# Kernel optimization log

Measured on AMD Instinct MI355X. Metric: run time of the kernel, lower is better.

## Reference

```python
import jax, jax.numpy as jnp
import numpy as np

E = 1024      # hidden_size
H = 16        # num_attention_heads
HD = E // H   # head_dim
EPS = 1e-5


def _mw_linear(x, Wt, bt, Wi, bi, split):
    # multiway linear: text weights on tokens [:split], image weights on [split:]
    xt = x[:, :split] @ Wt.T + bt
    xi = x[:, split:] @ Wi.T + bi
    return jnp.concatenate([xt, xi], axis=1)


def _ln(x, g, b):
    mu = jnp.mean(x, axis=-1, keepdims=True)
    var = jnp.mean(jnp.square(x - mu), axis=-1, keepdims=True)
    return (x - mu) * jax.lax.rsqrt(var + EPS) * g + b


def _mw_ln(x, gt, bt, gi, bi, split):
    return jnp.concatenate([_ln(x[:, :split], gt, bt), _ln(x[:, split:], gi, bi)], axis=1)


def setup_inputs() -> dict:
    key = jax.random.key(0)
    ks = jax.random.split(key, 24)
    B, T = 8, 1024
    d = {
        'query': jax.random.normal(ks[0], (B, T, E), jnp.float32),
        'key': jax.random.normal(ks[1], (B, T, E), jnp.float32),
        'value': jax.random.normal(ks[2], (B, T, E), jnp.float32),
        'attention_mask': jax.random.normal(ks[3], (T, T), jnp.float32) * 0.02,
    }
    i = 4
    for name in ['q', 'k', 'v', 'o']:
        d[f'W{name}_t'] = jax.random.normal(ks[i], (E, E), jnp.float32) * 0.02; i += 1
        d[f'b{name}_t'] = jnp.zeros((E,), jnp.float32)
        d[f'W{name}_i'] = jax.random.normal(ks[i], (E, E), jnp.float32) * 0.02; i += 1
        d[f'b{name}_i'] = jnp.zeros((E,), jnp.float32)
    d['ln_g_t'] = jnp.ones((E,), jnp.float32)
    d['ln_b_t'] = jnp.zeros((E,), jnp.float32)
    d['ln_g_i'] = jnp.ones((E,), jnp.float32)
    d['ln_b_i'] = jnp.zeros((E,), jnp.float32)
    d['split_position'] = 64
    return d


def reference(query, key, value, attention_mask,
              Wq_t, bq_t, Wq_i, bq_i,
              Wk_t, bk_t, Wk_i, bk_i,
              Wv_t, bv_t, Wv_i, bv_i,
              Wo_t, bo_t, Wo_i, bo_i,
              ln_g_t, ln_b_t, ln_g_i, ln_b_i,
              split_position):
    B, T, _ = query.shape
    S = key.shape[1]
    scaling = HD ** -0.5
    q = _mw_linear(query, Wq_t, bq_t, Wq_i, bq_i, split_position) * scaling
    k = _mw_linear(key, Wk_t, bk_t, Wk_i, bk_i, split_position)
    v = _mw_linear(value, Wv_t, bv_t, Wv_i, bv_i, split_position)
    q = q.reshape(B, T, H, HD)
    k = k.reshape(B, S, H, HD)
    v = v.reshape(B, S, H, HD)
    # [B, H, T, S] attention logits
    attn_weights = jnp.einsum('bthd,bshd->bhts', q, k)
    attn_weights = jnp.nan_to_num(attn_weights) + attention_mask[None, None]
    probs = jax.nn.softmax(attn_weights.astype(jnp.float32), axis=-1).astype(attn_weights.dtype)
    attn = jnp.einsum('bhts,bshd->bthd', probs, v).reshape(B, T, E)
    attn = _mw_ln(attn, ln_g_t, ln_b_t, ln_g_i, ln_b_i, split_position)
    attn = _mw_linear(attn, Wo_t, bo_t, Wo_i, bo_i, split_position)
    return attn
```

## Files before the change

kernel.cpp:

```cpp
#include <hip/hip_runtime.h>

#define E_DIM 1024
#define HEADS 16
#define HD 64
#define LOG2E 1.44269504088896340736f

typedef unsigned short ushort_t;
typedef __attribute__((ext_vector_type(8))) short bf16x8;
typedef __attribute__((ext_vector_type(4))) float floatx4;
typedef __attribute__((ext_vector_type(4))) float f32x4;
typedef __attribute__((ext_vector_type(16))) float floatx16;

__device__ inline unsigned int pack2bf(float a, float b) {
    unsigned int ua = __builtin_bit_cast(unsigned int, a);
    unsigned int ub = __builtin_bit_cast(unsigned int, b);
    ua = (ua + 0x8000u) >> 16;
    ub = (ub + 0x8000u) & 0xFFFF0000u;
    return ua | ub;
}
__device__ inline unsigned short f2bf(float a) {
    return (unsigned short)((__builtin_bit_cast(unsigned int, a) + 0x8000u) >> 16);
}
__device__ inline float bf2f(unsigned int s) {
    return __builtin_bit_cast(float, s << 16);
}

__device__ __forceinline__ void load_lds16(const void* g, void* l) {
    __builtin_amdgcn_global_load_lds(
        (const __attribute__((address_space(1))) unsigned int*)g,
        (__attribute__((address_space(3))) unsigned int*)l, 16, 0, 0);
}

__global__ __launch_bounds__(256) void cvt_inputs(
    const float* s0, const float* s1, const float* s2,
    ushort_t* d0, ushort_t* d1, ushort_t* d2)
{
    const float* __restrict__ src = (blockIdx.y == 0) ? s0 : (blockIdx.y == 1) ? s1 : s2;
    ushort_t* __restrict__ dst = (blockIdx.y == 0) ? d0 : (blockIdx.y == 1) ? d1 : d2;
    size_t i = ((size_t)blockIdx.x * 256 + threadIdx.x) * 8;
    float4 a = *(const float4*)&src[i];
    float4 b = *(const float4*)&src[i + 4];
    uint4 o;
    o.x = pack2bf(a.x, a.y); o.y = pack2bf(a.z, a.w);
    o.z = pack2bf(b.x, b.y); o.w = pack2bf(b.z, b.w);
    *(uint4*)&dst[i] = o;
}

__global__ __launch_bounds__(256) void cvt_weights(
    const float* w0, const float* w1, const float* w2, const float* w3,
    const float* w4, const float* w5, const float* w6, const float* w7,
    ushort_t* __restrict__ out)
{
    const float* srcs[8] = {w0, w1, w2, w3, w4, w5, w6, w7};
    const float* __restrict__ src = srcs[blockIdx.y];
    ushort_t* __restrict__ dst = out + (size_t)blockIdx.y * E_DIM * E_DIM;
    size_t i = ((size_t)blockIdx.x * 256 + threadIdx.x) * 8;
    float4 a = *(const float4*)&src[i];
    float4 b = *(const float4*)&src[i + 4];
    uint4 o;
    o.x = pack2bf(a.x, a.y); o.y = pack2bf(a.z, a.w);
    o.z = pack2bf(b.x, b.y); o.w = pack2bf(b.z, b.w);
    *(uint4*)&dst[i] = o;
}

__global__ __launch_bounds__(256) void mask_pack(
    const float* __restrict__ m, float* __restrict__ mp, int T_)
{
    int gid = blockIdx.x * 256 + threadIdx.x;
    int t  = gid >> 8;
    int s4 = (gid & 255) * 4;
    float4 v = *(const float4*)&m[(size_t)t * T_ + s4];
    int qt = t >> 5, q32 = t & 31;
    int it = s4 >> 6, s6 = s4 & 63;
    int j = s6 >> 5, up = (s6 >> 3) & 3, hi = (s6 >> 2) & 1;
    int L = j * 4 + up, lane = q32 + 32 * hi;
    size_t o = (((size_t)(qt * 16 + it) * 8 + L) * 64 + lane) * 4;
    float4 ov;
    ov.x = v.x * LOG2E - 16.0f; ov.y = v.y * LOG2E - 16.0f;
    ov.z = v.z * LOG2E - 16.0f; ov.w = v.w * LOG2E - 16.0f;
    *(float4*)&mp[o] = ov;
}

template<bool OUT_BF16>
__device__ __forceinline__ void gemm_core(
    const ushort_t* __restrict__ x, const ushort_t* __restrict__ W,
    const float* __restrict__ bias, void* __restrict__ outv,
    int m0, int n0, int split, int kind, float scale, int T_)
{
    __shared__ __align__(16) ushort_t As[2][128 * 32];
    __shared__ __align__(16) ushort_t Bs[2][128 * 32];

    const int tid  = threadIdx.x;
    const int lane = tid & 63;
    const int wv   = tid >> 6;
    const int rw   = (wv >> 1) * 64;
    const int cw   = (wv & 1) * 64;
    const int am   = lane & 15;
    const int aq   = lane >> 4;

    const int grow = wv * 32 + (lane >> 2);
    const int gcol = ((lane & 3) ^ ((lane >> 3) & 3)) * 8;
    const int akey = ((am >> 1) & 3) * 8;

    floatx4 acc[4][4];
    #pragma unroll
    for (int i = 0; i < 4; ++i)
        #pragma unroll
        for (int j = 0; j < 4; ++j)
            acc[i][j] = (floatx4){0.f, 0.f, 0.f, 0.f};

    load_lds16(&x[(size_t)(m0 + grow) * E_DIM + gcol],      &As[0][(wv * 32) * 32]);
    load_lds16(&x[(size_t)(m0 + grow + 16) * E_DIM + gcol], &As[0][(wv * 32 + 16) * 32]);
    load_lds16(&W[(size_t)(n0 + grow) * E_DIM + gcol],      &Bs[0][(wv * 32) * 32]);
    load_lds16(&W[(size_t)(n0 + grow + 16) * E_DIM + gcol], &Bs[0][(wv * 32 + 16) * 32]);
    __syncthreads();

    for (int k0 = 0; k0 < E_DIM; k0 += 32) {
        const int cur = (k0 >> 5) & 1;
        if (k0 + 32 < E_DIM) {
            const int nxt = cur ^ 1;
            const int kn  = k0 + 32;
            load_lds16(&x[(size_t)(m0 + grow) * E_DIM + kn + gcol],      &As[nxt][(wv * 32) * 32]);
            load_lds16(&x[(size_t)(m0 + grow + 16) * E_DIM + kn + gcol], &As[nxt][(wv * 32 + 16) * 32]);
            load_lds16(&W[(size_t)(n0 + grow) * E_DIM + kn + gcol],      &Bs[nxt][(wv * 32) * 32]);
            load_lds16(&W[(size_t)(n0 + grow + 16) * E_DIM + kn + gcol], &Bs[nxt][(wv * 32 + 16) * 32]);
        }

        bf16x8 af[4], bfv[4];
        #pragma unroll
        for (int i = 0; i < 4; ++i)
            af[i] = *(const bf16x8*)&As[cur][(rw + i * 16 + am) * 32 + ((aq * 8) ^ akey)];
        #pragma unroll
        for (int j = 0; j < 4; ++j)
            bfv[j] = *(const bf16x8*)&Bs[cur][(cw + j * 16 + am) * 32 + ((aq * 8) ^ akey)];

        #pragma unroll
        for (int i = 0; i < 4; ++i)
            #pragma unroll
            for (int j = 0; j < 4; ++j)
                acc[i][j] = __builtin_amdgcn_mfma_f32_16x16x32_bf16(af[i], bfv[j], acc[i][j], 0, 0, 0);

        __syncthreads();
    }

    const int cq = lane >> 4;
    const int cm = lane & 15;
    const int t0m = m0 % T_;
    #pragma unroll
    for (int j = 0; j < 4; ++j) {
        int n = n0 + cw + j * 16 + cm;
        float bv = bias[n];
        #pragma unroll
        for (int i = 0; i < 4; ++i) {
            int mbase = m0 + rw + i * 16 + cq * 4;
            int tbase = t0m + rw + i * 16 + cq * 4;
            #pragma unroll
            for (int r = 0; r < 4; ++r) {
                int m = mbase + r;
                int t = tbase + r;
                if (((t < split) ? 0 : 1) != kind) continue;
                float val = (acc[i][j][r] + bv) * scale;
                if (OUT_BF16) ((ushort_t*)outv)[(size_t)m * E_DIM + n] = f2bf(val);
                else          ((float*)outv)[(size_t)m * E_DIM + n] = val;
            }
        }
    }
}

__device__ __forceinline__ int gemm_pick_m0(int kind, int split, int T_, bool& ok)
{
    ok = true;
    if (kind == 0) {
        const int nq = (split + 127) >> 7;
        const int Bb = (int)(gridDim.x * 128) / T_;
        if ((int)blockIdx.x >= Bb * nq) { ok = false; return 0; }
        const int batch = blockIdx.x / nq, tq = blockIdx.x % nq;
        return batch * T_ + tq * 128;
    }
    const int m0 = blockIdx.x * 128;
    if ((m0 % T_) + 128 <= split) { ok = false; return 0; }
    return m0;
}

__global__ __launch_bounds__(256) void gemm_qkv(
    const ushort_t* __restrict__ xq, const ushort_t* __restrict__ xk,
    const ushort_t* __restrict__ xv, const ushort_t* __restrict__ wall,
    const float* bq_t, const float* bq_i, const float* bk_t, const float* bk_i,
    const float* bv_t, const float* bv_i,
    ushort_t* oq, ushort_t* ok, ushort_t* ov,
    const int* __restrict__ split_ptr, int T_)
{
    const int split = *split_ptr;
    const int z = blockIdx.z;
    const int op = z >> 1;
    const int kind = z & 1;
    const int n0 = blockIdx.y * 128;

    bool ok2;
    const int m0 = gemm_pick_m0(kind, split, T_, ok2);
    if (!ok2) return;

    const ushort_t* x = (op == 0) ? xq : (op == 1) ? xk : xv;
    ushort_t* outp    = (op == 0) ? oq : (op == 1) ? ok : ov;
    const ushort_t* W = wall + (size_t)z * E_DIM * E_DIM;
    const float* bias = (op == 0) ? (kind ? bq_i : bq_t)
                      : (op == 1) ? (kind ? bk_i : bk_t)
                                  : (kind ? bv_i : bv_t);
    float scale = (op == 0) ? 0.125f * LOG2E : 1.0f;

    gemm_core<true>(x, W, bias, outp, m0, n0, split, kind, scale, T_);
}

__global__ __launch_bounds__(256) void gemm_o(
    const ushort_t* __restrict__ x, const ushort_t* __restrict__ Wt,
    const float* bt, const ushort_t* __restrict__ Wi, const float* bi,
    float* __restrict__ outp, const int* __restrict__ split_ptr, int T_)
{
    const int split = *split_ptr;
    const int kind = blockIdx.z;
    const int n0 = blockIdx.y * 128;

    bool ok2;
    const int m0 = gemm_pick_m0(kind, split, T_, ok2);
    if (!ok2) return;

    gemm_core<false>(x, kind ? Wi : Wt, kind ? bi : bt, outp, m0, n0, split, kind, 1.0f, T_);
}

__global__ __launch_bounds__(256) void attn_mfma32(
    const ushort_t* __restrict__ q, const ushort_t* __restrict__ k,
    const ushort_t* __restrict__ v, const float* __restrict__ maskP,
    ushort_t* __restrict__ outp, int T_)
{
    const int tid  = threadIdx.x;
    const int lane = tid & 63;
    const int wv   = tid >> 6;
    const int b    = blockIdx.x;
    const int h    = blockIdx.y;
    const int r0   = blockIdx.z * 128;

    const int q32 = lane & 31;
    const int hi  = lane >> 5;

    __shared__ __align__(16) ushort_t Ks[64 * 72];
    __shared__ __align__(16) ushort_t VT[64 * 72];

    const int qrow = r0 + wv * 32 + q32;
    const int qt16 = ((r0 >> 5) + wv) * 16;

    bf16x8 aqf[4];
    #pragma unroll
    for (int dc = 0; dc < 4; ++dc)
        aqf[dc] = *(const bf16x8*)&q[((size_t)(b * T_ + qrow)) * E_DIM + h * HD + dc * 16 + hi * 8];

    floatx16 oa[2];
    #pragma unroll
    for (int n = 0; n < 2; ++n)
        #pragma unroll
        for (int i = 0; i < 16; ++i) oa[n][i] = 0.f;
    float lsum = 0.f;

    const int kr = tid >> 2;
    const int kc = (tid & 3) * 16;
    const int vr = (tid >> 4) * 4;
    const int vc = (tid & 15) * 4;

    uint4 kreg[2];
    uint2 vreg[4];

    kreg[0] = *(const uint4*)&k[((size_t)(b * T_ + kr)) * E_DIM + h * HD + kc];
    kreg[1] = *(const uint4*)&k[((size_t)(b * T_ + kr)) * E_DIM + h * HD + kc + 8];
    #pragma unroll
    for (int i = 0; i < 4; ++i)
        vreg[i] = *(const uint2*)&v[((size_t)(b * T_ + vr + i)) * E_DIM + h * HD + vc];

    *(uint4*)&Ks[kr * 72 + kc]     = kreg[0];
    *(uint4*)&Ks[kr * 72 + kc + 8] = kreg[1];
    {
        const ushort_t* vp = (const ushort_t*)vreg;
        #pragma unroll
        for (int t = 0; t < 4; ++t) {
            uint2 w;
            w.x = (unsigned int)vp[0 * 4 + t] | ((unsigned int)vp[1 * 4 + t] << 16);
            w.y = (unsigned int)vp[2 * 4 + t] | ((unsigned int)vp[3 * 4 + t] << 16);
            *(uint2*)&VT[(vc + t) * 72 + vr] = w;
        }
    }
    __syncthreads();

    const int NT = T_ / 64;
    #pragma unroll 1
    for (int it = 0; it < NT; ++it) {
        const int s0 = it * 64;

        if (it + 1 < NT) {
            const int sn = s0 + 64;
            kreg[0] = *(const uint4*)&k[((size_t)(b * T_ + sn + kr)) * E_DIM + h * HD + kc];
            kreg[1] = *(const uint4*)&k[((size_t)(b * T_ + sn + kr)) * E_DIM + h * HD + kc + 8];
            #pragma unroll
            for (int i = 0; i < 4; ++i)
                vreg[i] = *(const uint2*)&v[((size_t)(b * T_ + sn + vr + i)) * E_DIM + h * HD + vc];
        }

        f32x4 mk[8];
        {
            const float* mp = maskP + ((size_t)(qt16 + it) << 11) + (lane << 2);
            #pragma unroll
            for (int L = 0; L < 8; ++L)
                mk[L] = *(const f32x4*)&mp[L << 8];
        }

        floatx16 sa[2];
        #pragma unroll
        for (int j = 0; j < 2; ++j)
            #pragma unroll
            for (int i = 0; i < 16; ++i) sa[j][i] = 0.f;
        __builtin_amdgcn_s_setprio(1);
        #pragma unroll
        for (int j = 0; j < 2; ++j)
            #pragma unroll
            for (int dc = 0; dc < 4; ++dc) {
                bf16x8 kf = *(const bf16x8*)&Ks[(32 * j + q32) * 72 + dc * 16 + hi * 8];
                sa[j] = __builtin_amdgcn_mfma_f32_32x32x16_bf16(kf, aqf[dc], sa[j], 0, 0, 0);
            }
        __builtin_amdgcn_s_setprio(0);

        float lp0 = 0.f, lp1 = 0.f, lp2 = 0.f, lp3 = 0.f;
        #pragma unroll
        for (int j = 0; j < 2; ++j)
            #pragma unroll
            for (int i = 0; i < 16; ++i) {
                float e = exp2f(sa[j][i] + mk[(j << 2) | (i >> 2)][i & 3]);
                sa[j][i] = e;
                if ((i & 3) == 0) lp0 += e;
                else if ((i & 3) == 1) lp1 += e;
                else if ((i & 3) == 2) lp2 += e;
                else lp3 += e;
            }
        lsum += (lp0 + lp1) + (lp2 + lp3);

        unsigned int W[2][8], X[2][8];
        #pragma unroll
        for (int j = 0; j < 2; ++j)
            #pragma unroll
            for (int u = 0; u < 8; ++u)
                W[j][u] = pack2bf(sa[j][2 * u], sa[j][2 * u + 1]);
        #pragma unroll
        for (int j = 0; j < 2; ++j)
            #pragma unroll
            for (int u = 0; u < 8; ++u)
                X[j][u] = (unsigned int)__shfl_xor((int)W[j][u], 32, 64);

        __builtin_amdgcn_s_setprio(1);
        #pragma unroll
        for (int s = 0; s < 4; ++s) {
            const int j = s >> 1;
            const int hh = (s & 1) * 4;
            union { unsigned int u[4]; bf16x8 v8; } pf;
            pf.u[0] = hi ? X[j][hh + 2] : W[j][hh + 0];
            pf.u[1] = hi ? X[j][hh + 3] : W[j][hh + 1];
            pf.u[2] = hi ? W[j][hh + 2] : X[j][hh + 0];
            pf.u[3] = hi ? W[j][hh + 3] : X[j][hh + 1];
            #pragma unroll
            for (int n = 0; n < 2; ++n) {
                bf16x8 vf = *(const bf16x8*)&VT[(n * 32 + q32) * 72 + s * 16 + hi * 8];
                oa[n] = __builtin_amdgcn_mfma_f32_32x32x16_bf16(pf.v8, vf, oa[n], 0, 0, 0);
            }
        }
        __builtin_amdgcn_s_setprio(0);

        if (it + 1 < NT) {
            __syncthreads();
            *(uint4*)&Ks[kr * 72 + kc]     = kreg[0];
            *(uint4*)&Ks[kr * 72 + kc + 8] = kreg[1];
            const ushort_t* vp = (const ushort_t*)vreg;
            #pragma unroll
            for (int t = 0; t < 4; ++t) {
                uint2 w;
                w.x = (unsigned int)vp[0 * 4 + t] | ((unsigned int)vp[1 * 4 + t] << 16);
                w.y = (unsigned int)vp[2 * 4 + t] | ((unsigned int)vp[3 * 4 + t] << 16);
                *(uint2*)&VT[(vc + t) * 72 + vr] = w;
            }
            __syncthreads();
        }
    }

    lsum += __shfl_xor(lsum, 32, 64);
    float inv = 1.0f / lsum;
    #pragma unroll
    for (int i = 0; i < 16; ++i) {
        int qi = (i & 3) + 8 * (i >> 2) + 4 * hi;
        float vi = __shfl(inv, qi + (lane & 32), 64);
        size_t orow = ((size_t)(b * T_ + r0 + wv * 32 + qi)) * E_DIM + h * HD;
        outp[orow + q32]      = f2bf(oa[0][i] * vi);
        outp[orow + 32 + q32] = f2bf(oa[1][i] * vi);
    }
}

__global__ __launch_bounds__(256) void mw_ln_bf16(
    const ushort_t* __restrict__ x,
    const float* __restrict__ gt, const float* __restrict__ bt,
    const float* __restrict__ gi, const float* __restrict__ bi,
    ushort_t* __restrict__ out,
    const int* __restrict__ split_ptr, int T_)
{
    const int split = *split_ptr;
    const int row = blockIdx.x;
    const int t = row % T_;
    const float* __restrict__ g  = (t < split) ? gt : gi;
    const float* __restrict__ bb = (t < split) ? bt : bi;

    const int tid = threadIdx.x;
    const int lane = tid & 63;
    const int wid = tid >> 6;

    __shared__ float red[8];

    uint2 xv = *(const uint2*)&x[(size_t)row * E_DIM + tid * 4];
    float f0 = bf2f(xv.x & 0xffffu), f1 = bf2f(xv.x >> 16);
    float f2 = bf2f(xv.y & 0xffffu), f3 = bf2f(xv.y >> 16);
    float s = f0 + f1 + f2 + f3;
    #pragma unroll
    for (int off = 1; off < 64; off <<= 1) s += __shfl_xor(s, off, 64);
    if (lane == 0) red[wid] = s;
    __syncthreads();
    float mu = (red[0] + red[1] + red[2] + red[3]) * (1.0f / E_DIM);

    float d0 = f0 - mu, d1 = f1 - mu, d2 = f2 - mu, d3 = f3 - mu;
    float s2 = d0*d0 + d1*d1 + d2*d2 + d3*d3;
    #pragma unroll
    for (int off = 1; off < 64; off <<= 1) s2 += __shfl_xor(s2, off, 64);
    if (lane == 0) red[4 + wid] = s2;
    __syncthreads();
    float var = (red[4] + red[5] + red[6] + red[7]) * (1.0f / E_DIM);
    float rstd = rsqrtf(var + 1e-5f);

    float4 gv = *(const float4*)&g[tid * 4];
    float4 bv = *(const float4*)&bb[tid * 4];
    uint2 ov;
    ov.x = pack2bf(d0 * rstd * gv.x + bv.x, d1 * rstd * gv.y + bv.y);
    ov.y = pack2bf(d2 * rstd * gv.z + bv.z, d3 * rstd * gv.w + bv.w);
    *(uint2*)&out[(size_t)row * E_DIM + tid * 4] = ov;
}

extern "C" void kernel_launch(void* const* d_in, const int* in_sizes, int n_in,
                              void* d_out, int out_size, void* d_ws, size_t ws_size,
                              hipStream_t stream) {
    const float* query = (const float*)d_in[0];
    const float* key   = (const float*)d_in[1];
    const float* value = (const float*)d_in[2];
    const float* mask  = (const float*)d_in[3];
    const float* Wq_t = (const float*)d_in[4];  const float* bq_t = (const float*)d_in[5];
    const float* Wq_i = (const float*)d_in[6];  const float* bq_i = (const float*)d_in[7];
    const float* Wk_t = (const float*)d_in[8];  const float* bk_t = (const float*)d_in[9];
    const float* Wk_i = (const float*)d_in[10]; const float* bk_i = (const float*)d_in[11];
    const float* Wv_t = (const float*)d_in[12]; const float* bv_t = (const float*)d_in[13];
    const float* Wv_i = (const float*)d_in[14]; const float* bv_i = (const float*)d_in[15];
    const float* Wo_t = (const float*)d_in[16]; const float* bo_t = (const float*)d_in[17];
    const float* Wo_i = (const float*)d_in[18]; const float* bo_i = (const float*)d_in[19];
    const float* ln_g_t = (const float*)d_in[20]; const float* ln_b_t = (const float*)d_in[21];
    const float* ln_g_i = (const float*)d_in[22]; const float* ln_b_i = (const float*)d_in[23];
    const int* split = (const int*)d_in[24];

    float* out = (float*)d_out;

    const int BT = in_sizes[0] / E_DIM;
    const int T_ = 1024;
    const int B  = BT / T_;

    ushort_t* ws = (ushort_t*)d_ws;
    const size_t nx = (size_t)BT * E_DIM;
    const size_t nw = (size_t)E_DIM * E_DIM;
    ushort_t* xq_bf = ws;
    ushort_t* xk_bf = ws + nx;
    ushort_t* xv_bf = ws + 2 * nx;
    ushort_t* k_bf  = ws + 3 * nx;
    ushort_t* v_bf  = ws + 4 * nx;
    ushort_t* w_bf  = ws + 5 * nx;
    ushort_t* q_bf  = (ushort_t*)d_out;
    float* maskP    = (float*)xk_bf;

    dim3 blk(256);
    const int cvt_blocks = (int)(nx / 2048);
    const int wcvt_blocks = (int)(nw / 2048);

    cvt_weights<<<dim3(wcvt_blocks, 8), blk, 0, stream>>>(
        Wq_t, Wq_i, Wk_t, Wk_i, Wv_t, Wv_i, Wo_t, Wo_i, w_bf);
    cvt_inputs<<<dim3(cvt_blocks, 3), blk, 0, stream>>>(
        query, key, value, xq_bf, xk_bf, xv_bf);

    gemm_qkv<<<dim3(BT / 128, E_DIM / 128, 6), blk, 0, stream>>>(
        xq_bf, xk_bf, xv_bf, w_bf,
        bq_t, bq_i, bk_t, bk_i, bv_t, bv_i,
        q_bf, k_bf, v_bf, split, T_);

    mask_pack<<<dim3(T_ * T_ / 4 / 256), blk, 0, stream>>>(mask, maskP, T_);

    attn_mfma32<<<dim3(B, HEADS, T_ / 128), blk, 0, stream>>>(
        q_bf, k_bf, v_bf, maskP, q_bf, T_);

    mw_ln_bf16<<<dim3(BT), blk, 0, stream>>>(
        q_bf, ln_g_t, ln_b_t, ln_g_i, ln_b_i, xq_bf, split, T_);

    gemm_o<<<dim3(BT / 128, E_DIM / 128, 2), blk, 0, stream>>>(
        xq_bf, w_bf + 6 * nw, bo_t, w_bf + 7 * nw, bo_i, out, split, T_);
}
```

Measured before the change: 478.2 us.

## Fuse Q, K and V projections into a single GEMM block

Replaces the per-projection QKV GEMM (grid z=6) with one kernel in which each block computes the Q, K and V tiles for the same rows and columns. It keeps three accumulator sets and stages all three operand pairs into 96KB of dynamic LDS with double buffering. The aim is fewer blocks and shared index and launch setup. The cost is much higher register and LDS use per block, which lowers occupancy, and the three projections share no input data to reuse.

```diff
diff --git a/kernel.cpp b/kernel.cpp
--- a/kernel.cpp
+++ b/kernel.cpp
@@ -81,6 +81,135 @@
     *(float4*)&mp[o] = ov;
 }
 
+__device__ __forceinline__ int gemm_pick_m0(int kind, int split, int T_, bool& ok)
+{
+    ok = true;
+    if (kind == 0) {
+        const int nq = (split + 127) >> 7;
+        const int Bb = (int)(gridDim.x * 128) / T_;
+        if ((int)blockIdx.x >= Bb * nq) { ok = false; return 0; }
+        const int batch = blockIdx.x / nq, tq = blockIdx.x % nq;
+        return batch * T_ + tq * 128;
+    }
+    const int m0 = blockIdx.x * 128;
+    if ((m0 % T_) + 128 <= split) { ok = false; return 0; }
+    return m0;
+}
+
+__global__ __launch_bounds__(256) void gemm_qkv_f(
+    const ushort_t* __restrict__ xq, const ushort_t* __restrict__ xk,
+    const ushort_t* __restrict__ xv, const ushort_t* __restrict__ wall,
+    const float* bq_t, const float* bq_i, const float* bk_t, const float* bk_i,
+    const float* bv_t, const float* bv_i,
+    ushort_t* oq, ushort_t* ok, ushort_t* ov,
+    const int* __restrict__ split_ptr, int T_)
+{
+    extern __shared__ __align__(16) ushort_t sh[];
+
+    const int split = *split_ptr;
+    const int kind = blockIdx.z;
+    const int n0 = blockIdx.y * 128;
+    bool ok2;
+    const int m0 = gemm_pick_m0(kind, split, T_, ok2);
+    if (!ok2) return;
+
+    const int tid  = threadIdx.x;
+    const int lane = tid & 63;
+    const int wv   = tid >> 6;
+    const int rw   = (wv >> 1) * 64;
+    const int cw   = (wv & 1) * 64;
+    const int am   = lane & 15;
+    const int aq   = lane >> 4;
+
+    const int grow = wv * 32 + (lane >> 2);
+    const int gcol = ((lane & 3) ^ ((lane >> 3) & 3)) * 8;
+    const int akey = ((am >> 1) & 3) * 8;
+
+    const ushort_t* xp[3] = { xq, xk, xv };
+    const ushort_t* Wp[3] = { wall + (size_t)(0 * 2 + kind) * E_DIM * E_DIM,
+                              wall + (size_t)(1 * 2 + kind) * E_DIM * E_DIM,
+                              wall + (size_t)(2 * 2 + kind) * E_DIM * E_DIM };
+
+    ushort_t* As = sh;
+    ushort_t* Bs = sh + 24576;
+
+    floatx4 acc[3][4][4];
+    #pragma unroll
+    for (int op = 0; op < 3; ++op)
+        #pragma unroll
+        for (int i = 0; i < 4; ++i)
+            #pragma unroll
+            for (int j = 0; j < 4; ++j)
+                acc[op][i][j] = (floatx4){0.f, 0.f, 0.f, 0.f};
+
+    auto stage_all = [&](int kn, int buf) {
+        #pragma unroll
+        for (int op = 0; op < 3; ++op) {
+            ushort_t* a = As + (op * 2 + buf) * 4096;
+            ushort_t* b = Bs + (op * 2 + buf) * 4096;
+            load_lds16(&xp[op][(size_t)(m0 + grow) * E_DIM + kn + gcol],      &a[(wv * 32) * 32]);
+            load_lds16(&xp[op][(size_t)(m0 + grow + 16) * E_DIM + kn + gcol], &a[(wv * 32 + 16) * 32]);
+            load_lds16(&Wp[op][(size_t)(n0 + grow) * E_DIM + kn + gcol],      &b[(wv * 32) * 32]);
+            load_lds16(&Wp[op][(size_t)(n0 + grow + 16) * E_DIM + kn + gcol], &b[(wv * 32 + 16) * 32]);
+        }
+    };
+
+    stage_all(0, 0);
+    __syncthreads();
+
+    for (int k0 = 0; k0 < E_DIM; k0 += 32) {
+        const int cur = (k0 >> 5) & 1;
+        if (k0 + 32 < E_DIM)
+            stage_all(k0 + 32, cur ^ 1);
+
+        #pragma unroll
+        for (int op = 0; op < 3; ++op) {
+            const ushort_t* a = As + (op * 2 + cur) * 4096;
+            const ushort_t* b = Bs + (op * 2 + cur) * 4096;
+            bf16x8 af[4], bfv[4];
+            #pragma unroll
+            for (int i = 0; i < 4; ++i)
+                af[i] = *(const bf16x8*)&a[(rw + i * 16 + am) * 32 + ((aq * 8) ^ akey)];
+            #pragma unroll
+            for (int j = 0; j < 4; ++j)
+                bfv[j] = *(const bf16x8*)&b[(cw + j * 16 + am) * 32 + ((aq * 8) ^ akey)];
+            #pragma unroll
+            for (int i = 0; i < 4; ++i)
+                #pragma unroll
+                for (int j = 0; j < 4; ++j)
+                    acc[op][i][j] = __builtin_amdgcn_mfma_f32_16x16x32_bf16(af[i], bfv[j], acc[op][i][j], 0, 0, 0);
+        }
+        __syncthreads();
+    }
+
+    const int cq = lane >> 4;
+    const int cm = lane & 15;
+    const int t0m = m0 % T_;
+    const float* biases[3] = { kind ? bq_i : bq_t, kind ? bk_i : bk_t, kind ? bv_i : bv_t };
+    ushort_t* outs[3] = { oq, ok, ov };
+    #pragma unroll
+    for (int op = 0; op < 3; ++op) {
+        const float scale = (op == 0) ? 0.125f * LOG2E : 1.0f;
+        ushort_t* outp = outs[op];
+        #pragma unroll
+        for (int j = 0; j < 4; ++j) {
+            int n = n0 + cw + j * 16 + cm;
+            float bv = biases[op][n];
+            #pragma unroll
+            for (int i = 0; i < 4; ++i) {
+                int mbase = m0 + rw + i * 16 + cq * 4;
+                int tbase = t0m + rw + i * 16 + cq * 4;
+                #pragma unroll
+                for (int r = 0; r < 4; ++r) {
+                    int t = tbase + r;
+                    if (((t < split) ? 0 : 1) != kind) continue;
+                    outp[(size_t)(mbase + r) * E_DIM + n] = f2bf((acc[op][i][j][r] + bv) * scale);
+                }
+            }
+        }
+    }
+}
+
 template<bool OUT_BF16>
 __device__ __forceinline__ void gemm_core(
     const ushort_t* __restrict__ x, const ushort_t* __restrict__ W,
@@ -165,50 +294,6 @@
             }
         }
     }
-}
-
-__device__ __forceinline__ int gemm_pick_m0(int kind, int split, int T_, bool& ok)
-{
-    ok = true;
-    if (kind == 0) {
-        const int nq = (split + 127) >> 7;
-        const int Bb = (int)(gridDim.x * 128) / T_;
-        if ((int)blockIdx.x >= Bb * nq) { ok = false; return 0; }
-        const int batch = blockIdx.x / nq, tq = blockIdx.x % nq;
-        return batch * T_ + tq * 128;
-    }
-    const int m0 = blockIdx.x * 128;
-    if ((m0 % T_) + 128 <= split) { ok = false; return 0; }
-    return m0;
-}
-
-__global__ __launch_bounds__(256) void gemm_qkv(
-    const ushort_t* __restrict__ xq, const ushort_t* __restrict__ xk,
-    const ushort_t* __restrict__ xv, const ushort_t* __restrict__ wall,
-    const float* bq_t, const float* bq_i, const float* bk_t, const float* bk_i,
-    const float* bv_t, const float* bv_i,
-    ushort_t* oq, ushort_t* ok, ushort_t* ov,
-    const int* __restrict__ split_ptr, int T_)
-{
-    const int split = *split_ptr;
-    const int z = blockIdx.z;
-    const int op = z >> 1;
-    const int kind = z & 1;
-    const int n0 = blockIdx.y * 128;
-
-    bool ok2;
-    const int m0 = gemm_pick_m0(kind, split, T_, ok2);
-    if (!ok2) return;
-
-    const ushort_t* x = (op == 0) ? xq : (op == 1) ? xk : xv;
-    ushort_t* outp    = (op == 0) ? oq : (op == 1) ? ok : ov;
-    const ushort_t* W = wall + (size_t)z * E_DIM * E_DIM;
-    const float* bias = (op == 0) ? (kind ? bq_i : bq_t)
-                      : (op == 1) ? (kind ? bk_i : bk_t)
-                                  : (kind ? bv_i : bv_t);
-    float scale = (op == 0) ? 0.125f * LOG2E : 1.0f;
-
-    gemm_core<true>(x, W, bias, outp, m0, n0, split, kind, scale, T_);
 }
 
 __global__ __launch_bounds__(256) void gemm_o(
@@ -489,7 +574,7 @@
     cvt_inputs<<<dim3(cvt_blocks, 3), blk, 0, stream>>>(
         query, key, value, xq_bf, xk_bf, xv_bf);
 
-    gemm_qkv<<<dim3(BT / 128, E_DIM / 128, 6), blk, 0, stream>>>(
+    gemm_qkv_f<<<dim3(BT / 128, E_DIM / 128, 2), blk, 98304, stream>>>(
         xq_bf, xk_bf, xv_bf, w_bf,
         bq_t, bq_i, bk_t, bk_i, bv_t, bv_i,
         q_bf, k_bf, v_bf, split, T_);
```

Result: slower. 540.6 us (+13.0%).
